# Optimization experiments

Hardware: AMD Instinct MI355X
Metric: run time of the kernel (lower is better)

Reference implementation:

```python
import jax, jax.numpy as jnp
import numpy as np

N = 100_000      # num_nodes
E = 1_600_000    # num_edges (avg degree 16)
D = 64           # embedding_dim
L = 3            # num_layers


def setup_inputs() -> dict:
    key = jax.random.key(0)
    k1, k2 = jax.random.split(key)
    edge_index = jax.random.randint(k1, (2, E), 0, N, dtype=jnp.int64)
    edge_weight = jnp.ones((E,), jnp.float32)
    # nn.init.normal_(std=0.1)
    embedding = 0.1 * jax.random.normal(k2, (N, D), dtype=jnp.float32)
    return {"embedding": embedding, "edge_weight": edge_weight, "edge_index": edge_index}


def reference(embedding, edge_weight, edge_index):
    n = embedding.shape[0]
    self_idx = jnp.arange(n, dtype=edge_index.dtype)
    # add_self_loops: append (i, i) with weight 1 (PyG default fill_value)
    row = jnp.concatenate([edge_index[0], self_idx])  # source j
    col = jnp.concatenate([edge_index[1], self_idx])  # target i
    ew = jnp.concatenate([edge_weight, jnp.ones((n,), embedding.dtype)])
    # degree() counts occurrences of row (unweighted)
    deg = jax.ops.segment_sum(jnp.ones_like(ew), row, num_segments=n)
    deg_inv_sqrt = jnp.where(deg > 0, jax.lax.rsqrt(deg), 0.0)
    norm = deg_inv_sqrt[row] * ew * deg_inv_sqrt[col]  # [E+N]

    x = embedding
    acc = embedding  # running sum of layer-0..L embeddings
    for _ in range(L):
        # gather from source, scale, scatter-add to target (dropout off in eval)
        msg = norm[:, None] * x[row]                       # [E+N, D]
        x = jax.ops.segment_sum(msg, col, num_segments=n)  # [N, D]
        acc = acc + x
    return acc / (L + 1)
```

## Files before the change

### kernel.cpp

```cpp
#include <hip/hip_runtime.h>
#include <stdint.h>

#define DIM 64
#define BINS2 50000
#define RANGES 2
#define NSLICE 64
#define TBH 1024
#define SCAN_TILE 1024

__device__ __forceinline__ unsigned bf16rne(float f) {
    unsigned u = __float_as_uint(f);
    return (u + 0x7FFFu + ((u >> 16) & 1u)) >> 16;
}
__device__ __forceinline__ unsigned pack2(float lo, float hi) {
    return bf16rne(lo) | (bf16rne(hi) << 16);
}
#define UNPK(u, lo, hi) { lo = __uint_as_float((u) << 16); hi = __uint_as_float((u) & 0xFFFF0000u); }

__global__ void __launch_bounds__(TBH)
hist_kernel(const int* __restrict__ src, const int* __restrict__ dst,
            unsigned short* __restrict__ partialsA, unsigned short* __restrict__ partialsB,
            unsigned short* __restrict__ lrank, int E, int N, int Es) {
    __shared__ unsigned h32[BINS2 / 2];
    const int b = blockIdx.x;
    const int kind = b / (RANGES * NSLICE);
    const int rs = b % (RANGES * NSLICE);
    const int r = rs / NSLICE, s = rs % NSLICE;
    const int base = r * BINS2;
    const int hi = min(base + BINS2, N);
    const int nbw = (hi - base + 1) >> 1;
    for (int j = threadIdx.x; j < nbw; j += TBH) h32[j] = 0;
    __syncthreads();
    const int e0 = s * Es, e1 = min(e0 + Es, E);
    if (kind == 0) {
#pragma unroll 4
        for (int i = e0 + threadIdx.x; i < e1; i += TBH) {
            unsigned j = (unsigned)(dst[i] - base);
            if (j < (unsigned)BINS2) {
                const unsigned sh = (j & 1) * 16;
                unsigned old = atomicAdd(&h32[j >> 1], 1u << sh);
                lrank[i] = (unsigned short)((old >> sh) & 0xFFFFu);
            }
        }
    } else {
#pragma unroll 4
        for (int i = e0 + threadIdx.x; i < e1; i += TBH) {
            unsigned j = (unsigned)(src[i] - base);
            if (j < (unsigned)BINS2) atomicAdd(&h32[j >> 1], 1u << ((j & 1) * 16));
        }
    }
    __syncthreads();
    unsigned* part = (unsigned*)((kind ? partialsB : partialsA) + (size_t)s * N + base);
    for (int j = threadIdx.x; j < nbw; j += TBH) part[j] = h32[j];
}

__global__ void __launch_bounds__(256)
merge_kernel(unsigned short* __restrict__ partialsA, const unsigned short* __restrict__ partialsB,
             int* __restrict__ indeg, float* __restrict__ dis, int N) {
    const int i = blockIdx.x * blockDim.x + threadIdx.x;
    if (i >= N) return;
    int run = 0;
    for (int s = 0; s < NSLICE; ++s) {
        int v = partialsA[(size_t)s * N + i];
        partialsA[(size_t)s * N + i] = (unsigned short)run;
        run += v;
    }
    indeg[i] = run;
    int od = 0;
    for (int s = 0; s < NSLICE; ++s) od += partialsB[(size_t)s * N + i];
    dis[i] = rsqrtf((float)od + 1.0f);
}


__global__ void __launch_bounds__(256)
scan_partial(const int* __restrict__ indeg, int* __restrict__ partial, int n) {
    __shared__ int wsum[4];
    const int tid = threadIdx.x;
    const int base = blockIdx.x * SCAN_TILE + tid * 4;
    int s = 0;
    if (base + 3 < n) {
        int4 v = *(const int4*)(indeg + base);
        s = v.x + v.y + v.z + v.w;
    } else {
        for (int i = 0; i < 4; ++i) if (base + i < n) s += indeg[base + i];
    }
    for (int off = 32; off > 0; off >>= 1) s += __shfl_down(s, off, 64);
    const int lane = tid & 63, wid = tid >> 6;
    if (lane == 0) wsum[wid] = s;
    __syncthreads();
    if (tid == 0) partial[blockIdx.x] = wsum[0] + wsum[1] + wsum[2] + wsum[3];
}

__global__ void scan_blocksums(int* __restrict__ partial, int* __restrict__ offsets,
                               int nblocks, int n) {
    __shared__ int buf[1024];
    const int t = threadIdx.x;
    int v = (t < nblocks) ? partial[t] : 0;
    buf[t] = v;
    __syncthreads();
    for (int off = 1; off < 1024; off <<= 1) {
        int add = (t >= off) ? buf[t - off] : 0;
        __syncthreads();
        buf[t] += add;
        __syncthreads();
    }
    if (t < nblocks) partial[t] = buf[t] - v;
    if (t == 1023) offsets[n] = buf[1023];
}

__global__ void __launch_bounds__(256)
scan_final(const int* __restrict__ indeg, const int* __restrict__ partial,
           int* __restrict__ offsets, int n) {
    __shared__ int wpre[4];
    const int tid = threadIdx.x;
    const int base = blockIdx.x * SCAN_TILE + tid * 4;
    int v0 = 0, v1 = 0, v2 = 0, v3 = 0;
    if (base + 3 < n) {
        int4 v = *(const int4*)(indeg + base);
        v0 = v.x; v1 = v.y; v2 = v.z; v3 = v.w;
    } else {
        if (base + 0 < n) v0 = indeg[base + 0];
        if (base + 1 < n) v1 = indeg[base + 1];
        if (base + 2 < n) v2 = indeg[base + 2];
        if (base + 3 < n) v3 = indeg[base + 3];
    }
    const int s = v0 + v1 + v2 + v3;
    int inc = s;
    const int lane = tid & 63, wid = tid >> 6;
    for (int off = 1; off < 64; off <<= 1) {
        int t = __shfl_up(inc, off, 64);
        if (lane >= off) inc += t;
    }
    if (lane == 63) wpre[wid] = inc;
    __syncthreads();
    if (tid == 0) {
        int r = 0;
        for (int w = 0; w < 4; ++w) { int t = wpre[w]; wpre[w] = r; r += t; }
    }
    __syncthreads();
    int run = (inc - s) + wpre[wid] + partial[blockIdx.x];
    if (base + 0 < n) { offsets[base + 0] = run; run += v0; }
    if (base + 1 < n) { offsets[base + 1] = run; run += v1; }
    if (base + 2 < n) { offsets[base + 2] = run; run += v2; }
    if (base + 3 < n) { offsets[base + 3] = run; run += v3; }
}

__global__ void __launch_bounds__(256)
fill_kernel(const int* __restrict__ src, const int* __restrict__ dst,
            const float* __restrict__ ew, const float* __restrict__ dis,
            const int* __restrict__ offsets, const unsigned short* __restrict__ sliceoff,
            const unsigned short* __restrict__ lrank, int2* __restrict__ csr,
            int E, int N, int Es) {
    const int i0 = (blockIdx.x * blockDim.x + threadIdx.x) * 4;
    if (i0 + 3 < E) {
        int4   ss = *(const int4*)(src + i0);
        int4   tt = *(const int4*)(dst + i0);
        float4 ww = *(const float4*)(ew + i0);
        ushort4 lr = *(const ushort4*)(lrank + i0);
#define DO(K, SF, TF, WF, LF) { int sE = (i0 + K) / Es; \
        int slot = offsets[TF] + sliceoff[(size_t)sE * N + TF] + (int)(LF); \
        csr[slot] = make_int2(SF, __float_as_int(dis[SF] * (WF) * dis[TF])); }
        DO(0, ss.x, tt.x, ww.x, lr.x)
        DO(1, ss.y, tt.y, ww.y, lr.y)
        DO(2, ss.z, tt.z, ww.z, lr.z)
        DO(3, ss.w, tt.w, ww.w, lr.w)
#undef DO
    } else {
        for (int i = i0; i < E; ++i) {
            int sE = i / Es;
            int t = dst[i], sc = src[i];
            float w = dis[sc] * ew[i] * dis[t];
            int slot = offsets[t] + sliceoff[(size_t)sE * N + t] + (int)lrank[i];
            csr[slot] = make_int2(sc, __float_as_int(w));
        }
    }
}

__global__ void __launch_bounds__(256)
conv_kernel(const float4* __restrict__ in4, uint4* __restrict__ outb, int n8) {
    int i = blockIdx.x * blockDim.x + threadIdx.x;
    if (i >= n8) return;
    float4 a = in4[2 * i], b = in4[2 * i + 1];
    uint4 o;
    o.x = pack2(a.x, a.y); o.y = pack2(a.z, a.w);
    o.z = pack2(b.x, b.y); o.w = pack2(b.z, b.w);
    outb[i] = o;
}

__global__ void __launch_bounds__(256)
prop_kernel(const uint4* __restrict__ xg, const float4* __restrict__ selfF,
            uint4* __restrict__ xstore,
            const int* __restrict__ offsets, const int2* __restrict__ csr,
            const float* __restrict__ dis, int n) {
    const int lane = threadIdx.x & 63;
    const int fl  = lane & 7;
    const int sub = lane >> 3;
    const int wave = blockIdx.x * (blockDim.x >> 6) + (threadIdx.x >> 6);
    const int node = wave * 8 + sub;
    if (node >= n) return;

    const int beg = offsets[node];
    const int end = offsets[node + 1];
    const float d = dis[node];
    const float dd = d * d;

    float a0, a1, a2, a3, a4, a5, a6, a7;
    if (selfF) {
        float4 s0 = selfF[node * 16 + fl * 2];
        float4 s1 = selfF[node * 16 + fl * 2 + 1];
        a0 = dd * s0.x; a1 = dd * s0.y; a2 = dd * s0.z; a3 = dd * s0.w;
        a4 = dd * s1.x; a5 = dd * s1.y; a6 = dd * s1.z; a7 = dd * s1.w;
    } else {
        uint4 q = xg[(size_t)node * 8 + fl];
        float l, h;
        UNPK(q.x, l, h) a0 = dd * l; a1 = dd * h;
        UNPK(q.y, l, h) a2 = dd * l; a3 = dd * h;
        UNPK(q.z, l, h) a4 = dd * l; a5 = dd * h;
        UNPK(q.w, l, h) a6 = dd * l; a7 = dd * h;
    }

#define EDGE(E, Q) { float w_ = __int_as_float((E).y); float l, h; \
    UNPK((Q).x, l, h) a0 = fmaf(w_, l, a0); a1 = fmaf(w_, h, a1); \
    UNPK((Q).y, l, h) a2 = fmaf(w_, l, a2); a3 = fmaf(w_, h, a3); \
    UNPK((Q).z, l, h) a4 = fmaf(w_, l, a4); a5 = fmaf(w_, h, a5); \
    UNPK((Q).w, l, h) a6 = fmaf(w_, l, a6); a7 = fmaf(w_, h, a7); }

    int p = beg;
    for (; p + 8 <= end; p += 8) {
        int2 e0 = csr[p + 0], e1 = csr[p + 1], e2 = csr[p + 2], e3 = csr[p + 3];
        int2 e4 = csr[p + 4], e5 = csr[p + 5], e6 = csr[p + 6], e7 = csr[p + 7];
        uint4 q0 = xg[(size_t)e0.x * 8 + fl];
        uint4 q1 = xg[(size_t)e1.x * 8 + fl];
        uint4 q2 = xg[(size_t)e2.x * 8 + fl];
        uint4 q3 = xg[(size_t)e3.x * 8 + fl];
        uint4 q4 = xg[(size_t)e4.x * 8 + fl];
        uint4 q5 = xg[(size_t)e5.x * 8 + fl];
        uint4 q6 = xg[(size_t)e6.x * 8 + fl];
        uint4 q7 = xg[(size_t)e7.x * 8 + fl];
        EDGE(e0, q0) EDGE(e1, q1) EDGE(e2, q2) EDGE(e3, q3)
        EDGE(e4, q4) EDGE(e5, q5) EDGE(e6, q6) EDGE(e7, q7)
    }
    for (; p + 4 <= end; p += 4) {
        int2 e0 = csr[p + 0], e1 = csr[p + 1], e2 = csr[p + 2], e3 = csr[p + 3];
        uint4 q0 = xg[(size_t)e0.x * 8 + fl];
        uint4 q1 = xg[(size_t)e1.x * 8 + fl];
        uint4 q2 = xg[(size_t)e2.x * 8 + fl];
        uint4 q3 = xg[(size_t)e3.x * 8 + fl];
        EDGE(e0, q0) EDGE(e1, q1) EDGE(e2, q2) EDGE(e3, q3)
    }
    for (; p < end; ++p) {
        int2 e = csr[p];
        uint4 q = xg[(size_t)e.x * 8 + fl];
        EDGE(e, q)
    }
#undef EDGE

    uint4 o;
    o.x = pack2(a0, a1); o.y = pack2(a2, a3);
    o.z = pack2(a4, a5); o.w = pack2(a6, a7);
    xstore[(size_t)node * 8 + fl] = o;
}

__global__ void __launch_bounds__(256)
combine_kernel(const float4* __restrict__ emb4, const uint4* __restrict__ xa,
               const uint4* __restrict__ xb, const uint4* __restrict__ xc,
               float4* __restrict__ out4, int n8) {
    int i = blockIdx.x * blockDim.x + threadIdx.x;
    if (i >= n8) return;
    float4 e0 = emb4[2 * i], e1 = emb4[2 * i + 1];
    uint4 qa = xa[i], qb = xb[i], qc = xc[i];
    float r[8] = { e0.x, e0.y, e0.z, e0.w, e1.x, e1.y, e1.z, e1.w };
    float l, h;
    UNPK(qa.x, l, h) r[0] += l; r[1] += h;
    UNPK(qa.y, l, h) r[2] += l; r[3] += h;
    UNPK(qa.z, l, h) r[4] += l; r[5] += h;
    UNPK(qa.w, l, h) r[6] += l; r[7] += h;
    UNPK(qb.x, l, h) r[0] += l; r[1] += h;
    UNPK(qb.y, l, h) r[2] += l; r[3] += h;
    UNPK(qb.z, l, h) r[4] += l; r[5] += h;
    UNPK(qb.w, l, h) r[6] += l; r[7] += h;
    UNPK(qc.x, l, h) r[0] += l; r[1] += h;
    UNPK(qc.y, l, h) r[2] += l; r[3] += h;
    UNPK(qc.z, l, h) r[4] += l; r[5] += h;
    UNPK(qc.w, l, h) r[6] += l; r[7] += h;
    out4[2 * i]     = make_float4(0.25f * r[0], 0.25f * r[1], 0.25f * r[2], 0.25f * r[3]);
    out4[2 * i + 1] = make_float4(0.25f * r[4], 0.25f * r[5], 0.25f * r[6], 0.25f * r[7]);
}


extern "C" void kernel_launch(void* const* d_in, const int* in_sizes, int n_in,
                              void* d_out, int out_size, void* d_ws, size_t ws_size,
                              hipStream_t stream) {
    const float* emb = (const float*)d_in[0];
    const float* ew  = (const float*)d_in[1];
    const int*   ei  = (const int*)d_in[2];
    const int E = in_sizes[2] / 2;
    const int N = in_sizes[0] / DIM;
    const int* src = ei;
    const int* dst = ei + E;
    float* out = (float*)d_out;

    const int Es = (E + NSLICE - 1) / NSLICE;
    const int nscan = (N + SCAN_TILE - 1) / SCAN_TILE;

    char* w = (char*)d_ws;
    size_t partSz = ((size_t)NSLICE * N * 2 + 255) & ~(size_t)255;
    size_t xSz    = ((size_t)N * DIM * 2 + 255) & ~(size_t)255;
    size_t uSz    = (partSz > xSz) ? partSz : xSz;
    unsigned short* partialsA = (unsigned short*)w;
    uint4* xc = (uint4*)w; w += uSz;
    unsigned short* partialsB = (unsigned short*)w;
    uint4* xb = (uint4*)w; w += uSz;
    unsigned short* lrank = (unsigned short*)w; w += (size_t)E * 2;
    int* indeg   = (int*)w;  w += (size_t)N * 4;
    int* offsets = (int*)w;  w += (size_t)(N + 1) * 4;
    float* dis   = (float*)w; w += (size_t)N * 4;
    int* partial = (int*)w;  w += (size_t)1024 * 4;
    w = (char*)(((uintptr_t)w + 255) & ~(uintptr_t)255);
    int2* csr    = (int2*)w; w += (size_t)E * 8;
    w = (char*)(((uintptr_t)w + 255) & ~(uintptr_t)255);
    uint4* x0c   = (uint4*)w; w += xSz;
    uint4* xa    = (uint4*)w; w += xSz;

    const int TB = 256;
    hist_kernel<<<2 * RANGES * NSLICE, TBH, 0, stream>>>(src, dst, partialsA, partialsB,
                                                         lrank, E, N, Es);
    merge_kernel<<<(N + TB - 1) / TB, TB, 0, stream>>>(partialsA, partialsB,
                                                       indeg, dis, N);
    scan_partial<<<nscan, TB, 0, stream>>>(indeg, partial, N);
    scan_blocksums<<<1, 1024, 0, stream>>>(partial, offsets, nscan, N);
    scan_final<<<nscan, TB, 0, stream>>>(indeg, partial, offsets, N);
    const int e4 = (E + 3) / 4;
    fill_kernel<<<(e4 + TB - 1) / TB, TB, 0, stream>>>(src, dst, ew, dis, offsets,
                                                       partialsA, lrank, csr, E, N, Es);
    const int n8 = N * DIM / 8;
    conv_kernel<<<(n8 + TB - 1) / TB, TB, 0, stream>>>((const float4*)emb, x0c, n8);

    dim3 grid((N + 31) / 32), block(TB);
    prop_kernel<<<grid, block, 0, stream>>>(x0c, (const float4*)emb, xa,
                                            offsets, csr, dis, N);
    prop_kernel<<<grid, block, 0, stream>>>(xa, nullptr, xb,
                                            offsets, csr, dis, N);
    prop_kernel<<<grid, block, 0, stream>>>(xb, nullptr, xc,
                                            offsets, csr, dis, N);
    combine_kernel<<<(n8 + TB - 1) / TB, TB, 0, stream>>>((const float4*)emb, xa, xb, xc,
                                                          (float4*)out, n8);
}
```

Before: 284.8 us.

## Sort nodes by in-degree into a permutation to balance propagation waves

Adds a counting sort of nodes by in-degree (capped at 63): a histogram kernel, a 64-entry scan and an atomic placement kernel that fill a permutation array. Each propagation launch then processes nodes in permuted order, so the eight nodes sharing a wave have similar degrees and lanes diverge less in loop length. The cost is three extra small launches, a memset, and an indirect lookup per node. Because placement within a bucket is atomic, the node order is nondeterministic, which can make x-row writes and neighbour reads less coherent.

```diff
diff --git a/kernel.cpp b/kernel.cpp
--- a/kernel.cpp
+++ b/kernel.cpp
@@ -143,6 +143,34 @@
     if (base + 1 < n) { offsets[base + 1] = run; run += v1; }
     if (base + 2 < n) { offsets[base + 2] = run; run += v2; }
     if (base + 3 < n) { offsets[base + 3] = run; run += v3; }
+}
+
+
+__global__ void __launch_bounds__(256)
+deghist_kernel(const int* __restrict__ indeg, int* __restrict__ dhist, int N) {
+    int i = blockIdx.x * blockDim.x + threadIdx.x;
+    if (i < N) atomicAdd(&dhist[min(indeg[i], 63)], 1);
+}
+
+__global__ void degscan_kernel(const int* __restrict__ dhist, int* __restrict__ dcur) {
+    const int t = threadIdx.x;
+    int v = dhist[t];
+    int inc = v;
+    for (int off = 1; off < 64; off <<= 1) {
+        int u = __shfl_up(inc, off, 64);
+        if (t >= off) inc += u;
+    }
+    dcur[t] = inc - v;
+}
+
+__global__ void __launch_bounds__(256)
+place_perm(const int* __restrict__ indeg, int* __restrict__ dcur,
+           int* __restrict__ perm, int N) {
+    int i = blockIdx.x * blockDim.x + threadIdx.x;
+    if (i < N) {
+        int p = atomicAdd(&dcur[min(indeg[i], 63)], 1);
+        perm[p] = i;
+    }
 }
 
 __global__ void __launch_bounds__(256)
@@ -189,15 +217,16 @@
 
 __global__ void __launch_bounds__(256)
 prop_kernel(const uint4* __restrict__ xg, const float4* __restrict__ selfF,
-            uint4* __restrict__ xstore,
+            uint4* __restrict__ xstore, const int* __restrict__ perm,
             const int* __restrict__ offsets, const int2* __restrict__ csr,
             const float* __restrict__ dis, int n) {
     const int lane = threadIdx.x & 63;
     const int fl  = lane & 7;
     const int sub = lane >> 3;
     const int wave = blockIdx.x * (blockDim.x >> 6) + (threadIdx.x >> 6);
-    const int node = wave * 8 + sub;
-    if (node >= n) return;
+    const int g = wave * 8 + sub;
+    if (g >= n) return;
+    const int node = perm[g];
 
     const int beg = offsets[node];
     const int end = offsets[node + 1];
@@ -316,11 +345,16 @@
     int* offsets = (int*)w;  w += (size_t)(N + 1) * 4;
     float* dis   = (float*)w; w += (size_t)N * 4;
     int* partial = (int*)w;  w += (size_t)1024 * 4;
+    int* dhist   = (int*)w;  w += (size_t)64 * 4;
+    int* dcur    = (int*)w;  w += (size_t)64 * 4;
+    int* perm    = (int*)w;  w += (size_t)N * 4;
     w = (char*)(((uintptr_t)w + 255) & ~(uintptr_t)255);
     int2* csr    = (int2*)w; w += (size_t)E * 8;
     w = (char*)(((uintptr_t)w + 255) & ~(uintptr_t)255);
     uint4* x0c   = (uint4*)w; w += xSz;
     uint4* xa    = (uint4*)w; w += xSz;
+
+    hipMemsetAsync(dhist, 0, 64 * 4, stream);
 
     const int TB = 256;
     hist_kernel<<<2 * RANGES * NSLICE, TBH, 0, stream>>>(src, dst, partialsA, partialsB,
@@ -330,6 +364,11 @@
     scan_partial<<<nscan, TB, 0, stream>>>(indeg, partial, N);
     scan_blocksums<<<1, 1024, 0, stream>>>(partial, offsets, nscan, N);
     scan_final<<<nscan, TB, 0, stream>>>(indeg, partial, offsets, N);
+
+    deghist_kernel<<<(N + TB - 1) / TB, TB, 0, stream>>>(indeg, dhist, N);
+    degscan_kernel<<<1, 64, 0, stream>>>(dhist, dcur);
+    place_perm<<<(N + TB - 1) / TB, TB, 0, stream>>>(indeg, dcur, perm, N);
+
     const int e4 = (E + 3) / 4;
     fill_kernel<<<(e4 + TB - 1) / TB, TB, 0, stream>>>(src, dst, ew, dis, offsets,
                                                        partialsA, lrank, csr, E, N, Es);
@@ -337,11 +376,11 @@
     conv_kernel<<<(n8 + TB - 1) / TB, TB, 0, stream>>>((const float4*)emb, x0c, n8);
 
     dim3 grid((N + 31) / 32), block(TB);
-    prop_kernel<<<grid, block, 0, stream>>>(x0c, (const float4*)emb, xa,
+    prop_kernel<<<grid, block, 0, stream>>>(x0c, (const float4*)emb, xa, perm,
                                             offsets, csr, dis, N);
-    prop_kernel<<<grid, block, 0, stream>>>(xa, nullptr, xb,
+    prop_kernel<<<grid, block, 0, stream>>>(xa, nullptr, xb, perm,
                                             offsets, csr, dis, N);
-    prop_kernel<<<grid, block, 0, stream>>>(xb, nullptr, xc,
+    prop_kernel<<<grid, block, 0, stream>>>(xb, nullptr, xc, perm,
                                             offsets, csr, dis, N);
     combine_kernel<<<(n8 + TB - 1) / TB, TB, 0, stream>>>((const float4*)emb, xa, xb, xc,
                                                           (float4*)out, n8);
```

Result: slower. 848.7 us (+198.0%).
